# Optimization experiments

Measured on AMD Instinct MI355X. Metric: run time of the kernel, lower is better.

Reference implementation:

```python
import jax, jax.numpy as jnp
import numpy as np

N_NODES = 100000
N_EDGES = 1600000
D_IN = 128
D_HID = 128
D_OUT = 64


def setup_inputs() -> dict:
    key = jax.random.key(0)
    ks = jax.random.split(key, 8)
    x = jax.random.normal(ks[0], (N_NODES, D_IN), dtype=jnp.float32)
    edge_index = jax.random.randint(ks[1], (2, N_EDGES), 0, N_NODES, dtype=jnp.int64)
    s1 = 1.0 / np.sqrt(D_IN)
    s2 = 1.0 / np.sqrt(D_HID)
    W1 = jax.random.uniform(ks[2], (D_IN, D_HID), jnp.float32, -s1, s1)
    b1 = jnp.zeros((D_HID,), jnp.float32)
    W2 = jax.random.uniform(ks[3], (D_HID, D_HID), jnp.float32, -s2, s2)
    b2 = jnp.zeros((D_HID,), jnp.float32)
    fc_W = jax.random.uniform(ks[4], (D_HID, D_OUT), jnp.float32, -s2, s2)
    fc_b = jax.random.uniform(ks[5], (D_OUT,), jnp.float32, -s2, s2)
    return {"x": x, "edge_index": edge_index, "W1": W1, "b1": b1,
            "W2": W2, "b2": b2, "fc_W": fc_W, "fc_b": fc_b}


def _gcn_norm(edge_index, n_nodes):
    # add self-loops, compute symmetric normalization D^{-1/2} A D^{-1/2}
    loops = jnp.arange(n_nodes, dtype=edge_index.dtype)
    src = jnp.concatenate([edge_index[0], loops])  # [E+N]
    dst = jnp.concatenate([edge_index[1], loops])
    ones = jnp.ones(src.shape[0], jnp.float32)
    deg = jax.ops.segment_sum(ones, dst, num_segments=n_nodes)  # [N]
    dinv = 1.0 / jnp.sqrt(deg)  # deg >= 1 thanks to self-loops
    norm = dinv[src] * dinv[dst]  # [E+N]
    return src, dst, norm


def _gcn_conv(x, W, b, src, dst, norm, n_nodes):
    h = x @ W                                  # [N, d]
    msg = h[src] * norm[:, None]               # gather + scale, [E+N, d]
    out = jax.ops.segment_sum(msg, dst, num_segments=n_nodes)  # scatter-add
    return out + b


def reference(x, edge_index, W1, b1, W2, b2, fc_W, fc_b):
    n = x.shape[0]
    src, dst, norm = _gcn_norm(edge_index, n)
    h = jax.nn.relu(_gcn_conv(x, W1, b1, src, dst, norm, n))
    # dropout is identity in inference mode
    h = jax.nn.relu(_gcn_conv(h, W2, b2, src, dst, norm, n))
    return h @ fc_W + fc_b
```

## Files before the change

### kernel.cpp

```cpp
#include <hip/hip_runtime.h>

typedef __attribute__((ext_vector_type(8))) short bf16x8;
typedef __attribute__((ext_vector_type(4))) float f32x4;
typedef __attribute__((ext_vector_type(2))) float f32x2;

__device__ __forceinline__ unsigned short f2bf(float x) {
  union { float f; unsigned u; } v; v.f = x;
  return (unsigned short)((v.u + 0x7fffu + ((v.u >> 16) & 1u)) >> 16);
}
__device__ __forceinline__ float bf2f(unsigned short h) {
  union { unsigned u; float f; } v; v.u = ((unsigned)h) << 16; return v.f;
}


__global__ __launch_bounds__(256) void bhist_k(const int* __restrict__ dst,
                                               int* __restrict__ bcnt, int E, int B) {
  __shared__ int h[512];
  for (int i = threadIdx.x; i < B; i += 256) h[i] = 0;
  __syncthreads();
  for (int e = blockIdx.x * 256 + threadIdx.x; e < E; e += gridDim.x * 256)
    atomicAdd(&h[dst[e] >> 8], 1);
  __syncthreads();
  for (int i = threadIdx.x; i < B; i += 256)
    if (h[i]) atomicAdd(&bcnt[i * 16], h[i]);
}

__global__ __launch_bounds__(256) void bin_k(const int* __restrict__ src,
                                             const int* __restrict__ dst,
                                             const int* __restrict__ bcnt,
                                             int* __restrict__ bfill,
                                             unsigned* __restrict__ ebuf, int E, int B) {
  __shared__ int hist[512];
  __shared__ int base[512];
  __shared__ int sd[256];
  int t = threadIdx.x;
  int i0 = 2 * t, i1 = 2 * t + 1;
  int v0 = (i0 < B) ? bcnt[i0 * 16] : 0;
  int v1 = (i1 < B) ? bcnt[i1 * 16] : 0;
  int ts = v0 + v1;
  sd[t] = ts; __syncthreads();
  for (int off = 1; off < 256; off <<= 1) {
    int x = (t >= off) ? sd[t - off] : 0;
    __syncthreads();
    sd[t] += x;
    __syncthreads();
  }
  int excl = sd[t] - ts;
  base[i0] = excl;
  base[i1] = excl + v0;
  __syncthreads();

  int chunk = (E + gridDim.x - 1) / gridDim.x;
  int e0 = blockIdx.x * chunk;
  int e1 = e0 + chunk; if (e1 > E) e1 = E;
  for (int i = t; i < B; i += 256) hist[i] = 0;
  __syncthreads();
  for (int e = e0 + t; e < e1; e += 256) atomicAdd(&hist[dst[e] >> 8], 1);
  __syncthreads();
  for (int i = t; i < B; i += 256) {
    int c = hist[i];
    hist[i] = base[i] + (c ? atomicAdd(&bfill[i * 16], c) : 0);
  }
  __syncthreads();
  for (int e = e0 + t; e < e1; e += 256) {
    int d = dst[e];
    int b = d >> 8;
    int pos = atomicAdd(&hist[b], 1);
    ebuf[pos] = ((unsigned)(d & 255) << 17) | (unsigned)src[e];
  }
}

__global__ __launch_bounds__(256) void bsort_k(const unsigned* __restrict__ ebuf,
                                               const int* __restrict__ bcnt,
                                               int* __restrict__ csr,
                                               int* __restrict__ row_start,
                                               float* __restrict__ dinv, int N, int B, int E) {
  __shared__ int cnt[256];
  __shared__ int sd[256];
  __shared__ int ofs[256];
  __shared__ int sorted[8192];
  __shared__ int s_bs, s_m;
  int b = blockIdx.x, t = threadIdx.x;
  int i0 = 2 * t, i1 = 2 * t + 1;
  int v0 = (i0 < B) ? bcnt[i0 * 16] : 0;
  int v1 = (i1 < B) ? bcnt[i1 * 16] : 0;
  int ts = v0 + v1;
  sd[t] = ts; __syncthreads();
  for (int off = 1; off < 256; off <<= 1) {
    int x = (t >= off) ? sd[t - off] : 0;
    __syncthreads();
    sd[t] += x;
    __syncthreads();
  }
  int excl = sd[t] - ts;
  if (i0 == b) { s_bs = excl; s_m = v0; }
  if (i1 == b) { s_bs = excl + v0; s_m = v1; }
  if (b == 0 && t == 0) row_start[N] = E;
  __syncthreads();
  int bs = s_bs, m = s_m;
  if (m > 8192) m = 8192;

  cnt[t] = 0;
  __syncthreads();
  for (int i = t; i < m; i += 256) atomicAdd(&cnt[ebuf[bs + i] >> 17], 1);
  __syncthreads();
  int deg = cnt[t];
  sd[t] = deg; __syncthreads();
  for (int off = 1; off < 256; off <<= 1) {
    int x = (t >= off) ? sd[t - off] : 0;
    __syncthreads();
    sd[t] += x;
    __syncthreads();
  }
  int nexcl = sd[t] - deg;
  ofs[t] = nexcl;
  int node = (b << 8) + t;
  if (node < N) {
    row_start[node] = bs + nexcl;
    dinv[node] = rsqrtf((float)(deg + 1));
  }
  __syncthreads();
  for (int i = t; i < m; i += 256) {
    unsigned r = ebuf[bs + i];
    int d = r >> 17;
    int p = atomicAdd(&ofs[d], 1);
    if (p < 8192) sorted[p] = (int)(r & 0x1FFFFu);
  }
  __syncthreads();
  for (int i = t; i < m; i += 256) csr[bs + i] = sorted[i];
}

__global__ __launch_bounds__(256) void wfill_k(const int* __restrict__ csr,
                                               const float* __restrict__ dinv,
                                               int2* __restrict__ csrw, int E) {
  int e = blockIdx.x * 256 + threadIdx.x;
  if (e < E) {
    int s = csr[e];
    csrw[e] = make_int2(s, __float_as_int(dinv[s]));
  }
}

template <int NCOL, bool INF32, bool OUTF32>
__global__ __launch_bounds__(256) void gemm_k(const void* __restrict__ Ap,
                                              const float* __restrict__ W,
                                              const float* __restrict__ bias,
                                              void* __restrict__ Cp, int M) {
  __shared__ __align__(16) unsigned short Ws[NCOL * 136];
  int tid = threadIdx.x;
  for (int e = tid; e < 128 * NCOL; e += 256) {
    int k = e / NCOL, n = e % NCOL;
    Ws[n * 136 + k] = f2bf(W[e]);
  }
  __syncthreads();

  int wave = tid >> 6, lane = tid & 63;
  int q = lane >> 4, r = lane & 15;
  const int NT = NCOL / 16;
  int ntile = M >> 4;
  for (int tile = blockIdx.x * 4 + wave; tile < ntile; tile += gridDim.x * 4) {
    int row = tile * 16 + r;
    bf16x8 a[4];
    if (INF32) {
      const float* A = (const float*)Ap + (size_t)row * 128 + q * 8;
#pragma unroll
      for (int kk = 0; kk < 4; kk++) {
        const float4* p = (const float4*)(A + kk * 32);
        float4 f0 = p[0], f1 = p[1];
        bf16x8 tt;
        tt[0] = (short)f2bf(f0.x); tt[1] = (short)f2bf(f0.y);
        tt[2] = (short)f2bf(f0.z); tt[3] = (short)f2bf(f0.w);
        tt[4] = (short)f2bf(f1.x); tt[5] = (short)f2bf(f1.y);
        tt[6] = (short)f2bf(f1.z); tt[7] = (short)f2bf(f1.w);
        a[kk] = tt;
      }
    } else {
      const unsigned short* A = (const unsigned short*)Ap + (size_t)row * 128 + q * 8;
#pragma unroll
      for (int kk = 0; kk < 4; kk++) a[kk] = *(const bf16x8*)(A + kk * 32);
    }
    f32x4 acc[NT];
#pragma unroll
    for (int nt = 0; nt < NT; nt++) { acc[nt][0] = 0.f; acc[nt][1] = 0.f; acc[nt][2] = 0.f; acc[nt][3] = 0.f; }
#pragma unroll
    for (int kk = 0; kk < 4; kk++) {
#pragma unroll
      for (int nt = 0; nt < NT; nt++) {
        bf16x8 bfr = *(const bf16x8*)&Ws[(nt * 16 + r) * 136 + kk * 32 + q * 8];
        acc[nt] = __builtin_amdgcn_mfma_f32_16x16x32_bf16(a[kk], bfr, acc[nt], 0, 0, 0);
      }
    }
#pragma unroll
    for (int nt = 0; nt < NT; nt++) {
#pragma unroll
      for (int rr = 0; rr < 4; rr++) {
        int orow = tile * 16 + q * 4 + rr;
        int ocol = nt * 16 + r;
        if (OUTF32)
          ((float*)Cp)[(size_t)orow * NCOL + ocol] = acc[nt][rr] + bias[ocol];
        else
          ((unsigned short*)Cp)[(size_t)orow * NCOL + ocol] = f2bf(acc[nt][rr]);
      }
    }
  }
}

__global__ __launch_bounds__(256) void agg_k(const unsigned short* __restrict__ h,
                                             const float* __restrict__ dinv,
                                             const int* __restrict__ row_start,
                                             const int2* __restrict__ csrw,
                                             const float* __restrict__ bias,
                                             unsigned short* __restrict__ out, int N) {
  int lane = threadIdx.x & 63;
  int node = (blockIdx.x * 256 + threadIdx.x) >> 6;
  if (node >= N) return;
  int g = lane >> 4, r = lane & 15;
  float di = dinv[node];
  int beg = row_start[node];
  int deg = row_start[node + 1] - beg;

  f32x2 acc2[4];
#pragma unroll
  for (int i = 0; i < 4; i++) { acc2[i][0] = 0.f; acc2[i][1] = 0.f; }

#define ACC8(U, WV)                                                            \
  {                                                                            \
    f32x2 w2; w2[0] = (WV); w2[1] = (WV);                                      \
    f32x2 p0, p1, p2, p3;                                                      \
    p0[0] = __uint_as_float((U).x << 16);                                      \
    p0[1] = __uint_as_float((U).x & 0xffff0000u);                              \
    p1[0] = __uint_as_float((U).y << 16);                                      \
    p1[1] = __uint_as_float((U).y & 0xffff0000u);                              \
    p2[0] = __uint_as_float((U).z << 16);                                      \
    p2[1] = __uint_as_float((U).z & 0xffff0000u);                              \
    p3[0] = __uint_as_float((U).w << 16);                                      \
    p3[1] = __uint_as_float((U).w & 0xffff0000u);                              \
    acc2[0] += p0 * w2; acc2[1] += p1 * w2;                                    \
    acc2[2] += p2 * w2; acc2[3] += p3 * w2;                                    \
  }

  for (int base = -1; base < deg; base += 64) {
    int idx = base + lane;
    int s = node; float wv = 0.f;
    if (idx < 0) { wv = di; }
    else if (idx < deg) {
      int2 rec = csrw[beg + idx];
      s = rec.x; wv = __int_as_float(rec.y);
    }
    int cntv = deg - base; if (cntv > 64) cntv = 64;
    int j = 0;
    for (; j + 16 <= cntv; j += 16) {
      int s0 = __shfl(s, j + g);       float w0 = __shfl(wv, j + g);
      int s1 = __shfl(s, j + 4 + g);   float w1 = __shfl(wv, j + 4 + g);
      int s2 = __shfl(s, j + 8 + g);   float w2_ = __shfl(wv, j + 8 + g);
      int s3 = __shfl(s, j + 12 + g);  float w3 = __shfl(wv, j + 12 + g);
      uint4 u0 = *(const uint4*)(h + (size_t)s0 * 128 + r * 8);
      uint4 u1 = *(const uint4*)(h + (size_t)s1 * 128 + r * 8);
      uint4 u2 = *(const uint4*)(h + (size_t)s2 * 128 + r * 8);
      uint4 u3 = *(const uint4*)(h + (size_t)s3 * 128 + r * 8);
      ACC8(u0, w0); ACC8(u1, w1); ACC8(u2, w2_); ACC8(u3, w3);
    }
    for (; j < cntv; j += 4) {
      int sj = __shfl(s, j + g);
      float wj = __shfl(wv, j + g);
      uint4 u = *(const uint4*)(h + (size_t)sj * 128 + r * 8);
      ACC8(u, wj);
    }
  }
#undef ACC8

  float a[8];
#pragma unroll
  for (int d = 0; d < 4; d++) { a[2 * d] = acc2[d][0]; a[2 * d + 1] = acc2[d][1]; }
#pragma unroll
  for (int i = 0; i < 8; i++) {
    a[i] += __shfl_xor(a[i], 16);
    a[i] += __shfl_xor(a[i], 32);
  }

  if (g == 0) {
    bf16x8 t;
#pragma unroll
    for (int i = 0; i < 8; i++) {
      float v = a[i] * di + bias[r * 8 + i];
      if (v < 0.f) v = 0.f;
      t[i] = (short)f2bf(v);
    }
    *(bf16x8*)(out + (size_t)node * 128 + r * 8) = t;
  }
}

extern "C" void kernel_launch(void* const* d_in, const int* in_sizes, int n_in,
                              void* d_out, int out_size, void* d_ws, size_t ws_size,
                              hipStream_t stream) {
  const float* x  = (const float*)d_in[0];
  const int* ei   = (const int*)d_in[1];
  const float* W1 = (const float*)d_in[2];
  const float* b1 = (const float*)d_in[3];
  const float* W2 = (const float*)d_in[4];
  const float* b2 = (const float*)d_in[5];
  const float* fcW = (const float*)d_in[6];
  const float* fcb = (const float*)d_in[7];
  float* out = (float*)d_out;

  int N = in_sizes[0] / 128;
  int E = in_sizes[1] / 2;
  int B = (N + 255) >> 8;
  const int* src = ei;
  const int* dst = ei + E;

  char* w = (char*)d_ws;
  auto alloc = [&](size_t b) { char* p = w; w += (b + 255) & ~(size_t)255; return p; };
  float* dinv      = (float*)alloc((size_t)N * 4);
  int*   row_start = (int*)alloc((size_t)(N + 1) * 4);
  int*   batom     = (int*)alloc((size_t)(B + 1) * 128);
  int*   bcnt      = batom;
  int*   bfill     = batom + (size_t)(B + 1) * 16;
  unsigned* ebuf   = (unsigned*)alloc((size_t)E * 4);
  int*   csr       = (int*)alloc((size_t)E * 4);
  int2*  csrw      = (int2*)alloc((size_t)E * 8);
  unsigned short* bufA = (unsigned short*)alloc((size_t)N * 128 * 2);
  unsigned short* bufB = (unsigned short*)alloc((size_t)N * 128 * 2);

  hipMemsetAsync(batom, 0, (size_t)(B + 1) * 128, stream);

  bhist_k<<<256, 256, 0, stream>>>(dst, bcnt, E, B);
  bin_k<<<256, 256, 0, stream>>>(src, dst, bcnt, bfill, ebuf, E, B);
  bsort_k<<<B, 256, 0, stream>>>(ebuf, bcnt, csr, row_start, dinv, N, B, E);
  wfill_k<<<(E + 255) / 256, 256, 0, stream>>>(csr, dinv, csrw, E);

  gemm_k<128, true, false><<<512, 256, 0, stream>>>((const void*)x, W1, nullptr, (void*)bufA, N);
  agg_k<<<(N + 3) / 4, 256, 0, stream>>>(bufA, dinv, row_start, csrw, b1, bufB, N);
  gemm_k<128, false, false><<<512, 256, 0, stream>>>((const void*)bufB, W2, nullptr, (void*)bufA, N);
  agg_k<<<(N + 3) / 4, 256, 0, stream>>>(bufA, dinv, row_start, csrw, b2, bufB, N);
  gemm_k<64, false, true><<<512, 256, 0, stream>>>((const void*)bufB, fcW, fcb, (void*)out, N);
}
```

Before: 347.0 us.

## Pre-scale GEMM rows by dinv and drop per-edge weight array

The source-side normalization dinv[s] is folded into the GEMM epilogue, so each row of h is stored already scaled. Aggregation then only sums the gathered rows, which removes the wfill kernel, the 8-byte per-edge weight records and the weight shuffles, leaving 4-byte CSR indices. The inner loop is unrolled by 8 instead of 16, and a mask handles the tail. GEMM grid size also changes from 512 to 782 blocks. Rounding to bf16 now happens after the scale is applied, which slightly changes the numerics.

```diff
diff --git a/kernel.cpp b/kernel.cpp
--- a/kernel.cpp
+++ b/kernel.cpp
@@ -7,9 +7,6 @@
 __device__ __forceinline__ unsigned short f2bf(float x) {
   union { float f; unsigned u; } v; v.f = x;
   return (unsigned short)((v.u + 0x7fffu + ((v.u >> 16) & 1u)) >> 16);
-}
-__device__ __forceinline__ float bf2f(unsigned short h) {
-  union { unsigned u; float f; } v; v.u = ((unsigned)h) << 16; return v.f;
 }
 
 
@@ -130,20 +127,11 @@
   for (int i = t; i < m; i += 256) csr[bs + i] = sorted[i];
 }
 
-__global__ __launch_bounds__(256) void wfill_k(const int* __restrict__ csr,
-                                               const float* __restrict__ dinv,
-                                               int2* __restrict__ csrw, int E) {
-  int e = blockIdx.x * 256 + threadIdx.x;
-  if (e < E) {
-    int s = csr[e];
-    csrw[e] = make_int2(s, __float_as_int(dinv[s]));
-  }
-}
-
-template <int NCOL, bool INF32, bool OUTF32>
+template <int NCOL, bool INF32, bool OUTF32, bool SCALE>
 __global__ __launch_bounds__(256) void gemm_k(const void* __restrict__ Ap,
                                               const float* __restrict__ W,
                                               const float* __restrict__ bias,
+                                              const float* __restrict__ rowscale,
                                               void* __restrict__ Cp, int M) {
   __shared__ __align__(16) unsigned short Ws[NCOL * 136];
   int tid = threadIdx.x;
@@ -190,24 +178,25 @@
       }
     }
 #pragma unroll
-    for (int nt = 0; nt < NT; nt++) {
-#pragma unroll
-      for (int rr = 0; rr < 4; rr++) {
-        int orow = tile * 16 + q * 4 + rr;
+    for (int rr = 0; rr < 4; rr++) {
+      int orow = tile * 16 + q * 4 + rr;
+      float rs = SCALE ? rowscale[orow] : 1.f;
+#pragma unroll
+      for (int nt = 0; nt < NT; nt++) {
         int ocol = nt * 16 + r;
         if (OUTF32)
           ((float*)Cp)[(size_t)orow * NCOL + ocol] = acc[nt][rr] + bias[ocol];
         else
-          ((unsigned short*)Cp)[(size_t)orow * NCOL + ocol] = f2bf(acc[nt][rr]);
+          ((unsigned short*)Cp)[(size_t)orow * NCOL + ocol] = f2bf(acc[nt][rr] * rs);
       }
     }
   }
 }
 
-__global__ __launch_bounds__(256) void agg_k(const unsigned short* __restrict__ h,
+__global__ __launch_bounds__(256) void agg_k(const unsigned short* __restrict__ hs,
                                              const float* __restrict__ dinv,
                                              const int* __restrict__ row_start,
-                                             const int2* __restrict__ csrw,
+                                             const int* __restrict__ csr,
                                              const float* __restrict__ bias,
                                              unsigned short* __restrict__ out, int N) {
   int lane = threadIdx.x & 63;
@@ -222,51 +211,54 @@
 #pragma unroll
   for (int i = 0; i < 4; i++) { acc2[i][0] = 0.f; acc2[i][1] = 0.f; }
 
-#define ACC8(U, WV)                                                            \
+#define ACCADD(U)                                                              \
   {                                                                            \
-    f32x2 w2; w2[0] = (WV); w2[1] = (WV);                                      \
-    f32x2 p0, p1, p2, p3;                                                      \
-    p0[0] = __uint_as_float((U).x << 16);                                      \
-    p0[1] = __uint_as_float((U).x & 0xffff0000u);                              \
-    p1[0] = __uint_as_float((U).y << 16);                                      \
-    p1[1] = __uint_as_float((U).y & 0xffff0000u);                              \
-    p2[0] = __uint_as_float((U).z << 16);                                      \
-    p2[1] = __uint_as_float((U).z & 0xffff0000u);                              \
-    p3[0] = __uint_as_float((U).w << 16);                                      \
-    p3[1] = __uint_as_float((U).w & 0xffff0000u);                              \
-    acc2[0] += p0 * w2; acc2[1] += p1 * w2;                                    \
-    acc2[2] += p2 * w2; acc2[3] += p3 * w2;                                    \
+    f32x2 p;                                                                   \
+    p[0] = __uint_as_float((U).x << 16);                                       \
+    p[1] = __uint_as_float((U).x & 0xffff0000u); acc2[0] += p;                 \
+    p[0] = __uint_as_float((U).y << 16);                                       \
+    p[1] = __uint_as_float((U).y & 0xffff0000u); acc2[1] += p;                 \
+    p[0] = __uint_as_float((U).z << 16);                                       \
+    p[1] = __uint_as_float((U).z & 0xffff0000u); acc2[2] += p;                 \
+    p[0] = __uint_as_float((U).w << 16);                                       \
+    p[1] = __uint_as_float((U).w & 0xffff0000u); acc2[3] += p;                 \
+  }
+#define ACCFMA(U, M)                                                           \
+  {                                                                            \
+    f32x2 w2; w2[0] = (M); w2[1] = (M);                                        \
+    f32x2 p;                                                                   \
+    p[0] = __uint_as_float((U).x << 16);                                       \
+    p[1] = __uint_as_float((U).x & 0xffff0000u); acc2[0] += p * w2;            \
+    p[0] = __uint_as_float((U).y << 16);                                       \
+    p[1] = __uint_as_float((U).y & 0xffff0000u); acc2[1] += p * w2;            \
+    p[0] = __uint_as_float((U).z << 16);                                       \
+    p[1] = __uint_as_float((U).z & 0xffff0000u); acc2[2] += p * w2;            \
+    p[0] = __uint_as_float((U).w << 16);                                       \
+    p[1] = __uint_as_float((U).w & 0xffff0000u); acc2[3] += p * w2;            \
   }
 
   for (int base = -1; base < deg; base += 64) {
     int idx = base + lane;
-    int s = node; float wv = 0.f;
-    if (idx < 0) { wv = di; }
-    else if (idx < deg) {
-      int2 rec = csrw[beg + idx];
-      s = rec.x; wv = __int_as_float(rec.y);
-    }
+    int s = node;
+    if (idx >= 0 && idx < deg) s = csr[beg + idx];
     int cntv = deg - base; if (cntv > 64) cntv = 64;
     int j = 0;
-    for (; j + 16 <= cntv; j += 16) {
-      int s0 = __shfl(s, j + g);       float w0 = __shfl(wv, j + g);
-      int s1 = __shfl(s, j + 4 + g);   float w1 = __shfl(wv, j + 4 + g);
-      int s2 = __shfl(s, j + 8 + g);   float w2_ = __shfl(wv, j + 8 + g);
-      int s3 = __shfl(s, j + 12 + g);  float w3 = __shfl(wv, j + 12 + g);
-      uint4 u0 = *(const uint4*)(h + (size_t)s0 * 128 + r * 8);
-      uint4 u1 = *(const uint4*)(h + (size_t)s1 * 128 + r * 8);
-      uint4 u2 = *(const uint4*)(h + (size_t)s2 * 128 + r * 8);
-      uint4 u3 = *(const uint4*)(h + (size_t)s3 * 128 + r * 8);
-      ACC8(u0, w0); ACC8(u1, w1); ACC8(u2, w2_); ACC8(u3, w3);
+    for (; j + 8 <= cntv; j += 8) {
+      int s0 = __shfl(s, j + g);
+      int s1 = __shfl(s, j + 4 + g);
+      uint4 u0 = *(const uint4*)(hs + (size_t)s0 * 128 + r * 8);
+      uint4 u1 = *(const uint4*)(hs + (size_t)s1 * 128 + r * 8);
+      ACCADD(u0); ACCADD(u1);
     }
     for (; j < cntv; j += 4) {
       int sj = __shfl(s, j + g);
-      float wj = __shfl(wv, j + g);
-      uint4 u = *(const uint4*)(h + (size_t)sj * 128 + r * 8);
-      ACC8(u, wj);
-    }
-  }
-#undef ACC8
+      float mk = (j + g < cntv) ? 1.f : 0.f;
+      uint4 u = *(const uint4*)(hs + (size_t)sj * 128 + r * 8);
+      ACCFMA(u, mk);
+    }
+  }
+#undef ACCADD
+#undef ACCFMA
 
   float a[8];
 #pragma unroll
@@ -317,7 +309,6 @@
   int*   bfill     = batom + (size_t)(B + 1) * 16;
   unsigned* ebuf   = (unsigned*)alloc((size_t)E * 4);
   int*   csr       = (int*)alloc((size_t)E * 4);
-  int2*  csrw      = (int2*)alloc((size_t)E * 8);
   unsigned short* bufA = (unsigned short*)alloc((size_t)N * 128 * 2);
   unsigned short* bufB = (unsigned short*)alloc((size_t)N * 128 * 2);
 
@@ -326,11 +317,13 @@
   bhist_k<<<256, 256, 0, stream>>>(dst, bcnt, E, B);
   bin_k<<<256, 256, 0, stream>>>(src, dst, bcnt, bfill, ebuf, E, B);
   bsort_k<<<B, 256, 0, stream>>>(ebuf, bcnt, csr, row_start, dinv, N, B, E);
-  wfill_k<<<(E + 255) / 256, 256, 0, stream>>>(csr, dinv, csrw, E);
-
-  gemm_k<128, true, false><<<512, 256, 0, stream>>>((const void*)x, W1, nullptr, (void*)bufA, N);
-  agg_k<<<(N + 3) / 4, 256, 0, stream>>>(bufA, dinv, row_start, csrw, b1, bufB, N);
-  gemm_k<128, false, false><<<512, 256, 0, stream>>>((const void*)bufB, W2, nullptr, (void*)bufA, N);
-  agg_k<<<(N + 3) / 4, 256, 0, stream>>>(bufA, dinv, row_start, csrw, b2, bufB, N);
-  gemm_k<64, false, true><<<512, 256, 0, stream>>>((const void*)bufB, fcW, fcb, (void*)out, N);
-}
+
+  gemm_k<128, true, false, true><<<782, 256, 0, stream>>>((const void*)x, W1, nullptr, dinv,
+                                                          (void*)bufA, N);
+  agg_k<<<(N + 3) / 4, 256, 0, stream>>>(bufA, dinv, row_start, csr, b1, bufB, N);
+  gemm_k<128, false, false, true><<<782, 256, 0, stream>>>((const void*)bufB, W2, nullptr, dinv,
+                                                           (void*)bufA, N);
+  agg_k<<<(N + 3) / 4, 256, 0, stream>>>(bufA, dinv, row_start, csr, b2, bufB, N);
+  gemm_k<64, false, true, false><<<782, 256, 0, stream>>>((const void*)bufB, fcW, fcb, nullptr,
+                                                          (void*)out, N);
+}
```

Result: faster. 334.7 us (-3.5%).
